# Performance work log

Measured on AMD Instinct MI355X. Metric: run time of the kernel, lower is better.

## Reference

```python
import jax, jax.numpy as jnp
import numpy as np

EMBED = 1024
HEADS = 16
HEAD_DIM = EMBED // HEADS


def setup_inputs() -> dict:
    key = jax.random.key(0)
    ks = jax.random.split(key, 8)
    b, t, d = 2, 2048, EMBED
    s = 1.0 / np.sqrt(d)
    return {
        'k': jax.random.normal(ks[0], (b, t, d), jnp.float32),
        'q': jax.random.normal(ks[1], (b, t, d), jnp.float32),
        'v': jax.random.normal(ks[2], (b, t, d), jnp.float32),
        'Wk': jax.random.normal(ks[3], (d, d), jnp.float32) * s,
        'Wq': jax.random.normal(ks[4], (d, d), jnp.float32) * s,
        'Wv': jax.random.normal(ks[5], (d, d), jnp.float32) * s,
        'Wo': jax.random.normal(ks[6], (d, d), jnp.float32) * s,
        'bo': jax.random.normal(ks[7], (d,), jnp.float32) * 0.01,
    }


def reference(k, q, v, Wk, Wq, Wv, Wo, bo):
    b, t, d = q.shape
    h, n = HEADS, HEAD_DIM
    # projections (q_prj bias=False, k/v bias=False per add_bias_kv=False)
    keys = (k @ Wk.T).reshape(b, t, h, n).transpose(0, 2, 1, 3)      # b h t n
    queries = (q @ Wq.T).reshape(b, t, h, n).transpose(0, 2, 1, 3)
    values = (v @ Wv.T).reshape(b, t, h, n).transpose(0, 2, 1, 3)
    att = jnp.einsum('bhtn,bhsn->bhts', queries, keys)               # b h t t
    att = jax.nn.softmax(att / np.sqrt(n), axis=-1)
    out = jnp.einsum('bhts,bhsn->bhtn', att, values)                 # b h t n
    out = out.transpose(0, 2, 1, 3).reshape(b, t, d)                 # b t (h n)
    return out @ Wo.T + bo
```

## Files before the change

### kernel.cpp

```cpp
#include <hip/hip_runtime.h>
#include <hip/hip_bf16.h>


typedef unsigned short u16;
typedef unsigned int   u32;
using short8 = __attribute__((ext_vector_type(8))) short;
using f32x4  = __attribute__((ext_vector_type(4))) float;

__device__ __forceinline__ u16 f2b(float f) {
    u32 u = __float_as_uint(f);
    u += 0x7FFFu + ((u >> 16) & 1u);
    return (u16)(u >> 16);
}
__device__ __forceinline__ u32 pack2(float lo, float hi) {
    union { __hip_bfloat162 h; u32 u; } c;
    c.h = __float22bfloat162_rn(make_float2(lo, hi));
    return c.u;
}
__device__ __forceinline__ float fexp2(float x) {
    return __builtin_amdgcn_exp2f(x);
}
__device__ __forceinline__ void gld_lds16(const u16* g, u16* l) {
    __builtin_amdgcn_global_load_lds(
        (const __attribute__((address_space(1))) void*)g,
        (__attribute__((address_space(3))) void*)l, 16, 0, 0);
}

__global__ __launch_bounds__(256) void convert_kernel(
    const float* s0, const float* s1, const float* s2, const float* s3,
    const float* s4, const float* s5, const float* s6,
    u16* d0, u16* d1, u16* d2, u16* d3, u16* d4, u16* d5, u16* d6)
{
    const int y = blockIdx.y;
    const float* s; u16* d; u32 n;
    switch (y) {
        case 0: s = s0; d = d0; n = 1048576; break;
        case 1: s = s1; d = d1; n = 1048576; break;
        case 2: s = s2; d = d2; n = 1048576; break;
        case 3: s = s3; d = d3; n = 262144; break;
        case 4: s = s4; d = d4; n = 262144; break;
        case 5: s = s5; d = d5; n = 262144; break;
        default: s = s6; d = d6; n = 262144; break;
    }
    for (u32 i = blockIdx.x * 256 + threadIdx.x; i < n; i += 256 * 1024) {
        float4 f = ((const float4*)s)[i];
        uint2 o; o.x = pack2(f.x, f.y); o.y = pack2(f.z, f.w);
        ((uint2*)d)[i] = o;
    }
}

template <int MODE>
__device__ __forceinline__ void gemm_core(
    const u16* __restrict__ A, const u16* __restrict__ B,
    void* __restrict__ C, const float* __restrict__ bias, float scale,
    u32 bm, u32 bn)
{
    constexpr u32 K = 1024;
    __shared__ u16 As[128 * 32];
    __shared__ u16 Bs[128 * 32];

    const int tid  = threadIdx.x;
    const int lane = tid & 63;
    const int w    = tid >> 6;
    const int wr   = w >> 1, wc = w & 1;
    const int ml   = lane & 15, g = lane >> 4;

    f32x4 acc[4][4] = {};

    const u32 srow = w * 32 + (lane >> 2);
    const u32 scol = (u32)(((lane & 3) ^ ((lane >> 3) & 3)) * 8);
    const u16* gA = A + (size_t)(bm + srow) * K + scol;
    const u16* gB = B + (size_t)(bn + srow) * K + scol;
    u16* lA = &As[w * 1024];
    u16* lB = &Bs[w * 1024];

    const u32 fsw = (u32)((g ^ ((ml >> 1) & 3)) * 8);

    for (u32 k0 = 0; k0 < K; k0 += 32) {
        __syncthreads();
        gld_lds16(gA + k0, lA);
        gld_lds16(gA + 16 * K + k0, lA + 512);
        gld_lds16(gB + k0, lB);
        gld_lds16(gB + 16 * K + k0, lB + 512);
        __syncthreads();

        short8 af[4], bf[4];
#pragma unroll
        for (int it = 0; it < 4; ++it)
            af[it] = *(const short8*)&As[(wr * 64 + it * 16 + ml) * 32 + fsw];
#pragma unroll
        for (int ct = 0; ct < 4; ++ct)
            bf[ct] = *(const short8*)&Bs[(wc * 64 + ct * 16 + ml) * 32 + fsw];
#pragma unroll
        for (int it = 0; it < 4; ++it)
#pragma unroll
            for (int ct = 0; ct < 4; ++ct)
                acc[it][ct] = __builtin_amdgcn_mfma_f32_16x16x32_bf16(
                    af[it], bf[ct], acc[it][ct], 0, 0, 0);
    }

    if (MODE == 3) {
#pragma unroll
        for (int ct = 0; ct < 4; ++ct) {
            const u32 col = bn + wc * 64 + ct * 16 + ml;
            u16* dst = (u16*)C + (col >> 11) * 2097152 + (col & 2047);
#pragma unroll
            for (int it = 0; it < 4; ++it) {
                const u32 row = bm + wr * 64 + it * 16 + g * 4;
#pragma unroll
                for (int r = 0; r < 4; ++r)
                    dst[(size_t)(row + r) * 2048] = f2b(acc[it][ct][r]);
            }
        }
    } else {
#pragma unroll
        for (int ct = 0; ct < 4; ++ct) {
            const u32 col = bn + wc * 64 + ct * 16 + ml;
            const float bv = (MODE == 2 && bias) ? bias[col] : 0.0f;
#pragma unroll
            for (int it = 0; it < 4; ++it) {
                const u32 row = bm + wr * 64 + it * 16 + g * 4;
#pragma unroll
                for (int r = 0; r < 4; ++r) {
                    const float v = acc[it][ct][r] * scale + bv;
                    if (MODE == 2) ((float*)C)[(size_t)(row + r) * 1024 + col] = v;
                    else           ((u16*)C)[(size_t)(row + r) * 1024 + col] = f2b(v);
                }
            }
        }
    }
}

__global__ __launch_bounds__(256) void proj3_kernel(
    const u16* kb, const u16* qb, const u16* vb,
    const u16* Wkb, const u16* Wqb, const u16* Wvb,
    u16* Kp, u16* Qp, u16* Vt)
{
    if (blockIdx.z == 0)
        gemm_core<0>(kb, Wkb, Kp, nullptr, 1.0f, blockIdx.y * 128, blockIdx.x * 128);
    else if (blockIdx.z == 1)
        gemm_core<0>(qb, Wqb, Qp, nullptr, 0.18033688011112042f, blockIdx.y * 128, blockIdx.x * 128);
    else
        gemm_core<3>(Wvb, vb, Vt, nullptr, 1.0f, blockIdx.x * 128, blockIdx.y * 128);
}

__global__ __launch_bounds__(256) void out_gemm_kernel(
    const u16* __restrict__ A, const u16* __restrict__ W,
    float* __restrict__ C, const float* __restrict__ bias)
{
    constexpr u32 K = 1024;
    __shared__ u16 As[64 * 32];
    __shared__ u16 Bs[128 * 32];

    const int tid  = threadIdx.x;
    const int lane = tid & 63;
    const int w    = tid >> 6;
    const int wr   = w >> 1, wc = w & 1;
    const int ml   = lane & 15, g = lane >> 4;
    const u32 bm   = blockIdx.y * 64, bn = blockIdx.x * 128;

    f32x4 acc[2][4] = {};

    const u32 scol = (u32)(((lane & 3) ^ ((lane >> 3) & 3)) * 8);
    const u16* gA = A + (size_t)(bm + w * 16 + (lane >> 2)) * K + scol;
    const u16* gB = W + (size_t)(bn + w * 32 + (lane >> 2)) * K + scol;
    u16* lA = &As[w * 512];
    u16* lB = &Bs[w * 1024];

    const u32 fsw = (u32)((g ^ ((ml >> 1) & 3)) * 8);

    for (u32 k0 = 0; k0 < K; k0 += 32) {
        __syncthreads();
        gld_lds16(gA + k0, lA);
        gld_lds16(gB + k0, lB);
        gld_lds16(gB + 16 * K + k0, lB + 512);
        __syncthreads();

        short8 af[2], bf[4];
#pragma unroll
        for (int it = 0; it < 2; ++it)
            af[it] = *(const short8*)&As[(wr * 32 + it * 16 + ml) * 32 + fsw];
#pragma unroll
        for (int ct = 0; ct < 4; ++ct)
            bf[ct] = *(const short8*)&Bs[(wc * 64 + ct * 16 + ml) * 32 + fsw];
#pragma unroll
        for (int it = 0; it < 2; ++it)
#pragma unroll
            for (int ct = 0; ct < 4; ++ct)
                acc[it][ct] = __builtin_amdgcn_mfma_f32_16x16x32_bf16(
                    af[it], bf[ct], acc[it][ct], 0, 0, 0);
    }

#pragma unroll
    for (int ct = 0; ct < 4; ++ct) {
        const u32 col = bn + wc * 64 + ct * 16 + ml;
        const float bv = bias ? bias[col] : 0.0f;
#pragma unroll
        for (int it = 0; it < 2; ++it) {
            const u32 row = bm + wr * 32 + it * 16 + g * 4;
#pragma unroll
            for (int r = 0; r < 4; ++r)
                C[(size_t)(row + r) * 1024 + col] = acc[it][ct][r] + bv;
        }
    }
}

__global__ __launch_bounds__(256, 4) void attn_kernel(
    const u16* __restrict__ Qp, const u16* __restrict__ Kp,
    const u16* __restrict__ Vt, u16* __restrict__ Op)
{
    __shared__ u16   Ks[4096];
    __shared__ u16   Vs[4096];
    __shared__ u16   Ps[4 * 1280];
    __shared__ float Ls[2][32];

    const int tid  = threadIdx.x;
    const int lane = tid & 63;
    const int w    = tid >> 6;
    const int wq   = w >> 1;
    const int ws   = w & 1;
    const int ml   = lane & 15;
    const int g    = lane >> 4;
    const u32 bh   = blockIdx.y;
    const u32 b    = bh >> 4, h = bh & 15;
    const u32 t0   = blockIdx.x * 64;

    const u32 base  = b * 2048 * 1024 + h * 64;
    const u32 vbase = bh * 64 * 2048;

    short8 bq[2][2];
#pragma unroll
    for (int qt = 0; qt < 2; ++qt) {
        const u16* qr = Qp + base + (t0 + wq * 32 + qt * 16 + ml) * 1024 + g * 8;
        bq[qt][0] = *(const short8*)qr;
        bq[qt][1] = *(const short8*)(qr + 32);
    }

    f32x4 oacc[4][2] = {};
    float l4[2] = {};

    const u32 srow = (u32)(lane >> 3);
    const u32 schk = (u32)((lane & 7) ^ (lane >> 3));
    const u16* gK = Kp + base + (size_t)(w * 8 + srow) * 1024 + schk * 8;
    const u16* gV = Vt + vbase + (size_t)(w * 8 + srow) * 2048 + schk * 8;
    u16* lK0 = &Ks[w * 512];
    u16* lK1 = &Ks[2048 + w * 512];
    u16* lV0 = &Vs[w * 512];
    u16* lV1 = &Vs[2048 + w * 512];

    const u32 kaOff = (u32)((ws * 32 + ml) * 64 + ((g ^ (ml & 7)) * 8));
    const u32 vaOff = (u32)(ml * 64 + (((ws * 4 + g) ^ (ml & 7)) * 8));
    u16* Pw  = &Ps[w * 1280];
    u32* PwU = (u32*)Pw;
    const u32 pWr = (u32)(ml * 20 + g * 2);
    const u32 pRd = (u32)(ml * 40 + g * 8);

    for (int s = 0; s < 32; ++s) {
        __syncthreads();
        gld_lds16(gK, lK0);
        gld_lds16(gK + 32 * 1024, lK1);
        gld_lds16(gV, lV0);
        gld_lds16(gV + 32 * 2048, lV1);
        gK += 64 * 1024;
        gV += 64;
        __syncthreads();

        short8 vv[4];
#pragma unroll
        for (int dt = 0; dt < 4; ++dt)
            vv[dt] = *(const short8*)&Vs[vaOff + dt * 1024];

#pragma unroll
        for (int sub = 0; sub < 2; ++sub) {
            short8 k0 = *(const short8*)&Ks[kaOff + sub * 1024];
            short8 k1 = *(const short8*)&Ks[(kaOff ^ 32) + sub * 1024];
#pragma unroll
            for (int qt = 0; qt < 2; ++qt) {
                f32x4 z = {};
                z = __builtin_amdgcn_mfma_f32_16x16x32_bf16(k0, bq[qt][0], z, 0, 0, 0);
                z = __builtin_amdgcn_mfma_f32_16x16x32_bf16(k1, bq[qt][1], z, 0, 0, 0);
                const float p0 = fexp2(z[0]), p1 = fexp2(z[1]);
                const float p2 = fexp2(z[2]), p3 = fexp2(z[3]);
                l4[qt] += (p0 + p1) + (p2 + p3);
                uint2 pv; pv.x = pack2(p0, p1); pv.y = pack2(p2, p3);
                *(uint2*)&PwU[pWr + (u32)(qt * 320 + sub * 8)] = pv;
            }
        }

#pragma unroll
        for (int qt = 0; qt < 2; ++qt) {
            short8 pb = *(const short8*)&Pw[pRd + (u32)(qt * 640)];
#pragma unroll
            for (int dt = 0; dt < 4; ++dt)
                oacc[dt][qt] = __builtin_amdgcn_mfma_f32_16x16x32_bf16(
                    vv[dt], pb, oacc[dt][qt], 0, 0, 0);
        }
    }

#pragma unroll
    for (int qt = 0; qt < 2; ++qt) {
        l4[qt] += __shfl_xor(l4[qt], 16);
        l4[qt] += __shfl_xor(l4[qt], 32);
    }

    __syncthreads();
    float* Rw = (wq == 0) ? (float*)Ks : (float*)Vs;
    if (ws == 1) {
#pragma unroll
        for (int dt = 0; dt < 4; ++dt)
#pragma unroll
            for (int qt = 0; qt < 2; ++qt)
#pragma unroll
                for (int r = 0; r < 4; ++r)
                    Rw[(dt * 16 + g * 4 + r) * 32 + qt * 16 + ml] = oacc[dt][qt][r];
        if (g == 0) {
#pragma unroll
            for (int qt = 0; qt < 2; ++qt) Ls[wq][qt * 16 + ml] = l4[qt];
        }
    }
    __syncthreads();
    if (ws == 0) {
#pragma unroll
        for (int dt = 0; dt < 4; ++dt)
#pragma unroll
            for (int qt = 0; qt < 2; ++qt)
#pragma unroll
                for (int r = 0; r < 4; ++r)
                    oacc[dt][qt][r] += Rw[(dt * 16 + g * 4 + r) * 32 + qt * 16 + ml];
#pragma unroll
        for (int qt = 0; qt < 2; ++qt) {
            const u32 q = (u32)(wq * 32 + qt * 16 + ml);
            const float inv = 1.0f / (l4[qt] + Ls[wq][qt * 16 + ml]);
            const u32 row = (b * 2048 + t0 + q) * 1024 + h * 64;
#pragma unroll
            for (int dt = 0; dt < 4; ++dt) {
                const u32 ci = row + dt * 16 + g * 4;
                *(u32*)&Op[ci]     = pack2(oacc[dt][qt][0] * inv, oacc[dt][qt][1] * inv);
                *(u32*)&Op[ci + 2] = pack2(oacc[dt][qt][2] * inv, oacc[dt][qt][3] * inv);
            }
        }
    }
}

extern "C" void kernel_launch(void* const* d_in, const int* in_sizes, int n_in,
                              void* d_out, int out_size, void* d_ws, size_t ws_size,
                              hipStream_t stream)
{
    const float* kin = (const float*)d_in[0];
    const float* qin = (const float*)d_in[1];
    const float* vin = (const float*)d_in[2];
    const float* Wk  = (const float*)d_in[3];
    const float* Wq  = (const float*)d_in[4];
    const float* Wv  = (const float*)d_in[5];
    const float* Wo  = (const float*)d_in[6];
    const float* bo  = (const float*)d_in[7];
    float* out = (float*)d_out;

    const size_t ACT = 4194304;
    const size_t WSZ = 1048576;

    u16* kb  = (u16*)d_ws;
    u16* qb  = kb + ACT;
    u16* vb  = qb + ACT;
    u16* Wkb = vb + ACT;
    u16* Wqb = Wkb + WSZ;
    u16* Wvb = Wqb + WSZ;
    u16* Wob = Wvb + WSZ;
    u16* Kp  = Wob + WSZ;
    u16* Qp  = Kp + ACT;
    u16* Vt  = Qp + ACT;
    u16* Op  = kb;

    convert_kernel<<<dim3(1024, 7), 256, 0, stream>>>(
        kin, qin, vin, Wk, Wq, Wv, Wo, kb, qb, vb, Wkb, Wqb, Wvb, Wob);
    proj3_kernel<<<dim3(8, 32, 3), 256, 0, stream>>>(
        kb, qb, vb, Wkb, Wqb, Wvb, Kp, Qp, Vt);
    attn_kernel<<<dim3(32, 32), 256, 0, stream>>>(Qp, Kp, Vt, Op);
    out_gemm_kernel<<<dim3(8, 64), 256, 0, stream>>>(Op, Wob, out, bo);
}
```

Measured before the change: 214.3 us.

## Double-buffer K/V tiles in attention with 512-thread blocks and swizzled grid

The attention kernel moves to 512-thread blocks that each cover 128 query rows, so each K/V tile loaded into LDS feeds twice as many queries. K/V staging is double-buffered so the load of the next tile overlaps compute on the current one, which halves the barriers per tile. Block indices are remapped to schedule the work in a different order. The cost is more LDS per block and possibly lower occupancy; the epilogue reduction layout and the removed barrier before reusing Ks/Vs both need to be correct.

```diff
diff --git a/kernel.cpp b/kernel.cpp
--- a/kernel.cpp
+++ b/kernel.cpp
@@ -205,14 +205,14 @@
     }
 }
 
-__global__ __launch_bounds__(256, 4) void attn_kernel(
+__global__ __launch_bounds__(512, 4) void attn_kernel(
     const u16* __restrict__ Qp, const u16* __restrict__ Kp,
     const u16* __restrict__ Vt, u16* __restrict__ Op)
 {
-    __shared__ u16   Ks[4096];
-    __shared__ u16   Vs[4096];
-    __shared__ u16   Ps[4 * 1280];
-    __shared__ float Ls[2][32];
+    __shared__ u16   Ks[2 * 4096];
+    __shared__ u16   Vs[2 * 4096];
+    __shared__ u16   Ps[8 * 1280];
+    __shared__ float Ls[4][32];
 
     const int tid  = threadIdx.x;
     const int lane = tid & 63;
@@ -221,9 +221,12 @@
     const int ws   = w & 1;
     const int ml   = lane & 15;
     const int g    = lane >> 4;
-    const u32 bh   = blockIdx.y;
+
+    const u32 fid  = blockIdx.x + (blockIdx.y << 4);
+    const u32 swz  = (fid & 7) * 64 + (fid >> 3);
+    const u32 bh   = swz >> 4;
+    const u32 t0   = (swz & 15) * 128;
     const u32 b    = bh >> 4, h = bh & 15;
-    const u32 t0   = blockIdx.x * 64;
 
     const u32 base  = b * 2048 * 1024 + h * 64;
     const u32 vbase = bh * 64 * 2048;
@@ -244,9 +247,9 @@
     const u16* gK = Kp + base + (size_t)(w * 8 + srow) * 1024 + schk * 8;
     const u16* gV = Vt + vbase + (size_t)(w * 8 + srow) * 2048 + schk * 8;
     u16* lK0 = &Ks[w * 512];
-    u16* lK1 = &Ks[2048 + w * 512];
+    u16* lK1 = &Ks[4096 + w * 512];
     u16* lV0 = &Vs[w * 512];
-    u16* lV1 = &Vs[2048 + w * 512];
+    u16* lV1 = &Vs[4096 + w * 512];
 
     const u32 kaOff = (u32)((ws * 32 + ml) * 64 + ((g ^ (ml & 7)) * 8));
     const u32 vaOff = (u32)(ml * 64 + (((ws * 4 + g) ^ (ml & 7)) * 8));
@@ -255,47 +258,57 @@
     const u32 pWr = (u32)(ml * 20 + g * 2);
     const u32 pRd = (u32)(ml * 40 + g * 8);
 
-    for (int s = 0; s < 32; ++s) {
-        __syncthreads();
-        gld_lds16(gK, lK0);
-        gld_lds16(gK + 32 * 1024, lK1);
-        gld_lds16(gV, lV0);
-        gld_lds16(gV + 32 * 2048, lV1);
-        gK += 64 * 1024;
-        gV += 64;
-        __syncthreads();
-
-        short8 vv[4];
-#pragma unroll
-        for (int dt = 0; dt < 4; ++dt)
-            vv[dt] = *(const short8*)&Vs[vaOff + dt * 1024];
-
-#pragma unroll
-        for (int sub = 0; sub < 2; ++sub) {
-            short8 k0 = *(const short8*)&Ks[kaOff + sub * 1024];
-            short8 k1 = *(const short8*)&Ks[(kaOff ^ 32) + sub * 1024];
-#pragma unroll
-            for (int qt = 0; qt < 2; ++qt) {
-                f32x4 z = {};
-                z = __builtin_amdgcn_mfma_f32_16x16x32_bf16(k0, bq[qt][0], z, 0, 0, 0);
-                z = __builtin_amdgcn_mfma_f32_16x16x32_bf16(k1, bq[qt][1], z, 0, 0, 0);
-                const float p0 = fexp2(z[0]), p1 = fexp2(z[1]);
-                const float p2 = fexp2(z[2]), p3 = fexp2(z[3]);
-                l4[qt] += (p0 + p1) + (p2 + p3);
-                uint2 pv; pv.x = pack2(p0, p1); pv.y = pack2(p2, p3);
-                *(uint2*)&PwU[pWr + (u32)(qt * 320 + sub * 8)] = pv;
-            }
-        }
-
-#pragma unroll
-        for (int qt = 0; qt < 2; ++qt) {
-            short8 pb = *(const short8*)&Pw[pRd + (u32)(qt * 640)];
-#pragma unroll
-            for (int dt = 0; dt < 4; ++dt)
-                oacc[dt][qt] = __builtin_amdgcn_mfma_f32_16x16x32_bf16(
-                    vv[dt], pb, oacc[dt][qt], 0, 0, 0);
-        }
-    }
+#define ATTN_STAGE(KD, VD)                                                   \
+    { gld_lds16(gK, (KD)); gld_lds16(gV, (VD)); gK += 65536; gV += 64; }
+
+#define ATTN_COMPUTE(KB, VB)                                                 \
+    {                                                                        \
+        short8 vv[4];                                                        \
+        _Pragma("unroll")                                                    \
+        for (int dt = 0; dt < 4; ++dt)                                       \
+            vv[dt] = *(const short8*)&(VB)[vaOff + dt * 1024];               \
+        _Pragma("unroll")                                                    \
+        for (int sub = 0; sub < 2; ++sub) {                                  \
+            short8 k0 = *(const short8*)&(KB)[kaOff + sub * 1024];           \
+            short8 k1 = *(const short8*)&(KB)[(kaOff ^ 32) + sub * 1024];    \
+            _Pragma("unroll")                                                \
+            for (int qt = 0; qt < 2; ++qt) {                                 \
+                f32x4 z = {};                                                \
+                z = __builtin_amdgcn_mfma_f32_16x16x32_bf16(                 \
+                    k0, bq[qt][0], z, 0, 0, 0);                              \
+                z = __builtin_amdgcn_mfma_f32_16x16x32_bf16(                 \
+                    k1, bq[qt][1], z, 0, 0, 0);                              \
+                const float p0 = fexp2(z[0]), p1 = fexp2(z[1]);              \
+                const float p2 = fexp2(z[2]), p3 = fexp2(z[3]);              \
+                l4[qt] += (p0 + p1) + (p2 + p3);                             \
+                uint2 pv; pv.x = pack2(p0, p1); pv.y = pack2(p2, p3);        \
+                *(uint2*)&PwU[pWr + (u32)(qt * 320 + sub * 8)] = pv;         \
+            }                                                                \
+        }                                                                    \
+        _Pragma("unroll")                                                    \
+        for (int qt = 0; qt < 2; ++qt) {                                     \
+            short8 pb = *(const short8*)&Pw[pRd + (u32)(qt * 640)];          \
+            _Pragma("unroll")                                                \
+            for (int dt = 0; dt < 4; ++dt)                                   \
+                oacc[dt][qt] = __builtin_amdgcn_mfma_f32_16x16x32_bf16(      \
+                    vv[dt], pb, oacc[dt][qt], 0, 0, 0);                      \
+        }                                                                    \
+    }
+
+    ATTN_STAGE(lK0, lV0)
+    __syncthreads();
+
+#pragma unroll 1
+    for (int it = 0; it < 16; ++it) {
+        ATTN_STAGE(lK1, lV1)
+        ATTN_COMPUTE(Ks, Vs)
+        __syncthreads();
+        if (it < 15) ATTN_STAGE(lK0, lV0)
+        ATTN_COMPUTE(Ks + 4096, Vs + 4096)
+        __syncthreads();
+    }
+#undef ATTN_STAGE
+#undef ATTN_COMPUTE
 
 #pragma unroll
     for (int qt = 0; qt < 2; ++qt) {
@@ -303,8 +316,7 @@
         l4[qt] += __shfl_xor(l4[qt], 32);
     }
 
-    __syncthreads();
-    float* Rw = (wq == 0) ? (float*)Ks : (float*)Vs;
+    float* Rw = (wq < 2) ? ((float*)Ks + wq * 2048) : ((float*)Vs + (wq - 2) * 2048);
     if (ws == 1) {
 #pragma unroll
         for (int dt = 0; dt < 4; ++dt)
@@ -375,6 +387,6 @@
         kin, qin, vin, Wk, Wq, Wv, Wo, kb, qb, vb, Wkb, Wqb, Wvb, Wob);
     proj3_kernel<<<dim3(8, 32, 3), 256, 0, stream>>>(
         kb, qb, vb, Wkb, Wqb, Wvb, Kp, Qp, Vt);
-    attn_kernel<<<dim3(32, 32), 256, 0, stream>>>(Qp, Kp, Vt, Op);
+    attn_kernel<<<dim3(16, 32), 512, 0, stream>>>(Qp, Kp, Vt, Op);
     out_gemm_kernel<<<dim3(8, 64), 256, 0, stream>>>(Op, Wob, out, bo);
 }
```

Result: no change. 211.9 us (-1.1%).
